# Performance work log

Measured on AMD Instinct MI355X. Metric: run time of the kernel, lower is better.

Reference implementation:

```python
import jax, jax.numpy as jnp
import numpy as np


def setup_inputs() -> dict:
    key = jax.random.key(0)
    ks = jax.random.split(key, 8)
    B, C, H, W = 16, 192, 64, 64
    dt_rank, d_state = 12, 1
    return {
        "x": jax.random.normal(ks[0], (B, C, H, W), dtype=jnp.float32),
        "conv_w": jax.random.normal(ks[1], (C, 1, 5, 5), dtype=jnp.float32) * 0.1,
        "conv_b": jax.random.normal(ks[2], (C,), dtype=jnp.float32) * 0.1,
        "x_proj_w": jax.random.normal(ks[3], (dt_rank + 2 * d_state, C), dtype=jnp.float32) * (C ** -0.5),
        "dt_w": jax.random.normal(ks[4], (C, dt_rank), dtype=jnp.float32) * (dt_rank ** -0.5),
        "dt_b": jax.random.normal(ks[5], (C,), dtype=jnp.float32) * 0.1,
        "A_logs": jnp.zeros((C, d_state), dtype=jnp.float32),  # log(arange(1,d_state+1)) with d_state=1 -> 0
        "Ds": jnp.ones((C,), dtype=jnp.float32),
    }


def reference(x, conv_w, conv_b, x_proj_w, dt_w, dt_b, A_logs, Ds):
    B, C, H, W = x.shape
    L = H * W
    dt_rank = dt_w.shape[1]
    n = A_logs.shape[1]  # d_state
    # depthwise conv2d, kernel 5, padding SAME (=d_conv//2), then SiLU
    x = jax.lax.conv_general_dilated(
        x, conv_w, window_strides=(1, 1), padding='SAME',
        feature_group_count=C, dimension_numbers=('NCHW', 'OIHW', 'NCHW'))
    x = jax.nn.silu(x + conv_b[None, :, None, None])
    xs = x.reshape(B, C, L)  # (b, d, l)
    # x_proj: (dt_rank + 2n, C) @ (b, C, l)
    x_dbl = jnp.einsum('kc,bcl->bkl', x_proj_w, xs)
    dts, Bs, Cs = jnp.split(x_dbl, [dt_rank, dt_rank + n], axis=1)
    # dt projection + softplus (delta_softplus=True with delta_bias)
    delta = jax.nn.softplus(jnp.einsum('cr,brl->bcl', dt_w, dts) + dt_b[None, :, None])  # (b,d,l)
    A = -jnp.exp(A_logs)  # (d, n)
    # selective scan returning the full state trajectory h_t (b,d,n,l):
    # h_t = exp(delta_t * A) * h_{t-1} + delta_t * B_t * u_t
    a = jnp.exp(delta[:, :, None, :] * A[None, :, :, None])        # (b,d,n,l)
    b_el = delta[:, :, None, :] * Bs[:, None, :, :] * xs[:, :, None, :]  # (b,d,n,l)

    def combine(e1, e2):
        a1, b1 = e1
        a2, b2 = e2
        return (a1 * a2, a2 * b1 + b2)

    _, h = jax.lax.associative_scan(combine, (a, b_el), axis=-1)  # h: (b,d,n,l)
    state = h.reshape(B, C * n, L)
    # y = C_t * h_t + D * u (fp32, d_state=1 broadcast)
    y = state.astype(jnp.float32) * Cs.astype(jnp.float32) + xs * Ds[:, None]
    return y.reshape(B, C, H, W)
```

## Files before the change

kernel.cpp:

```cpp
#include <hip/hip_runtime.h>
#include <hip/hip_bf16.h>
#include <cstddef>

#define BB 16
#define CC 192
#define HH 64
#define WW 64
#define LL 4096
#define DTR 12
#define KK 14

__device__ __forceinline__ float silu_f(float v) {
  return v / (1.f + __expf(-v));
}

__global__ __launch_bounds__(256) void conv_silu_kernel(
    const float* __restrict__ x, const float* __restrict__ cw,
    const float* __restrict__ cb, float* __restrict__ xs) {
  const int bc = blockIdx.x;
  const int c = bc % CC;
  const int tid = threadIdx.x;
  const int lane = tid & 63;
  const int wv = tid >> 6;
  const int oy0 = wv * 16;

  float w[25];
#pragma unroll
  for (int k = 0; k < 25; ++k) w[k] = cw[c * 25 + k];
  const float bias = cb[c];

  const float* xp = x + (size_t)bc * LL + lane;
  float* op = xs + (size_t)bc * LL + lane;

  float rv[20];
#pragma unroll
  for (int r = 0; r < 20; ++r) {
    const int gr = oy0 + r - 2;
    float v = 0.f;
    if ((unsigned)gr < 64u) v = xp[gr * 64];
    rv[r] = v;
  }

  float acc[5];
#pragma unroll
  for (int i = 0; i < 5; ++i) acc[i] = 0.f;

#pragma unroll
  for (int r = 0; r < 20; ++r) {
    float v = rv[r];
    float vm2 = __shfl_up(v, 2u, 64);
    float vm1 = __shfl_up(v, 1u, 64);
    float vp1 = __shfl_down(v, 1u, 64);
    float vp2 = __shfl_down(v, 2u, 64);
    if (lane < 2) vm2 = 0.f;
    if (lane < 1) vm1 = 0.f;
    if (lane > 62) vp1 = 0.f;
    if (lane > 61) vp2 = 0.f;
    float t[5] = {vm2, vm1, v, vp1, vp2};
#pragma unroll
    for (int ky = 0; ky < 5; ++ky) {
      if (r >= ky && (r - ky) < 16) {
        float s = acc[(r - ky) % 5];
#pragma unroll
        for (int kx = 0; kx < 5; ++kx) s += w[ky * 5 + kx] * t[kx];
        acc[(r - ky) % 5] = s;
      }
    }
    if (r >= 4) {
      const int yf = oy0 + r - 4;
      float a = acc[(r - 4) % 5] + bias;
      op[yf * 64] = silu_f(a);
      acc[(r - 4) % 5] = 0.f;
    }
  }
}

__global__ __launch_bounds__(896) void proj_kernel(
    const float* __restrict__ xs, const float* __restrict__ xpw,
    float* __restrict__ xdbl) {
  const int b = blockIdx.y;
  const int l0 = blockIdx.x * 128;
  const int tid = threadIdx.x;
  const int lane = tid & 63;
  const int k = tid >> 6;

  const float* bp = xs + (size_t)b * CC * LL + l0 + lane * 2;
  const float* wp = xpw + k * CC;
  float ax = 0.f, ay = 0.f;
#pragma unroll 8
  for (int c = 0; c < CC; ++c) {
    const float2 v = *(const float2*)(bp + (size_t)c * LL);
    const float w = wp[c];
    ax += w * v.x;
    ay += w * v.y;
  }
  *(float2*)(xdbl + ((size_t)b * KK + k) * LL + l0 + lane * 2) =
      make_float2(ax, ay);
}

__global__ __launch_bounds__(512) void scan_kernel(
    const float* __restrict__ xs, const float* __restrict__ xdbl,
    const float* __restrict__ dtw, const float* __restrict__ dtb,
    const float* __restrict__ A_logs, const float* __restrict__ Ds,
    float* __restrict__ y) {
  const int bc = blockIdx.x;
  const int b = bc / CC;
  const int c = bc - b * CC;
  const int tid = threadIdx.x;
  const int lane = tid & 63;
  const int wv = tid >> 6;

  const float Ac = -__expf(A_logs[c]);
  const float Dc = Ds[c];
  float dw[DTR];
#pragma unroll
  for (int r = 0; r < DTR; ++r) dw[r] = dtw[c * DTR + r];
  const float db = dtb[c];

  const float* xp = xs + (size_t)bc * LL;
  const float* xb = xdbl + (size_t)b * KK * LL;
  float* yp = y + (size_t)bc * LL;

  __shared__ float segA[8];
  __shared__ float segB[8];

  float alpha[8], beta[8];
  float aggA[2], aggB[2];

#pragma unroll
  for (int ck = 0; ck < 2; ++ck) {
    const int base = wv * 512 + ck * 256 + lane * 4;
    const float4 x4 = *(const float4*)(xp + base);
    const float4 B4 = *(const float4*)(xb + 12 * LL + base);
    const float4 C4 = *(const float4*)(xb + 13 * LL + base);
    float zx = db, zy = db, zz_ = db, zw = db;
#pragma unroll
    for (int r = 0; r < DTR; ++r) {
      const float4 d4 = *(const float4*)(xb + r * LL + base);
      zx += dw[r] * d4.x;
      zy += dw[r] * d4.y;
      zz_ += dw[r] * d4.z;
      zw += dw[r] * d4.w;
    }
    const float zq[4] = {zx, zy, zz_, zw};
    float Pl = 1.f, hl = 0.f;
#pragma unroll
    for (int q = 0; q < 4; ++q) {
      const float z = zq[q];
      const float delta = (z > 15.f) ? z : __logf(1.f + __expf(z));
      const float a = __expf(delta * Ac);
      const float be = delta * ((&B4.x)[q]) * ((&x4.x)[q]);
      hl = a * hl + be;
      Pl = Pl * a;
      alpha[ck * 4 + q] = Pl * ((&C4.x)[q]);
      beta[ck * 4 + q] = hl * ((&C4.x)[q]) + ((&x4.x)[q]) * Dc;
    }
    aggA[ck] = Pl;
    aggB[ck] = hl;
  }

  float iA[2], iB[2];
#pragma unroll
  for (int ck = 0; ck < 2; ++ck) { iA[ck] = aggA[ck]; iB[ck] = aggB[ck]; }
#pragma unroll
  for (int s = 1; s < 64; s <<= 1) {
    float pA[2], pB[2];
#pragma unroll
    for (int ck = 0; ck < 2; ++ck) {
      pA[ck] = __shfl_up(iA[ck], (unsigned)s, 64);
      pB[ck] = __shfl_up(iB[ck], (unsigned)s, 64);
    }
    if (lane >= s) {
#pragma unroll
      for (int ck = 0; ck < 2; ++ck) {
        iB[ck] = iA[ck] * pB[ck] + iB[ck];
        iA[ck] = iA[ck] * pA[ck];
      }
    }
  }
  float eA[2], eB[2], tA[2], tB[2];
#pragma unroll
  for (int ck = 0; ck < 2; ++ck) {
    eA[ck] = __shfl_up(iA[ck], 1u, 64);
    eB[ck] = __shfl_up(iB[ck], 1u, 64);
    if (lane == 0) { eA[ck] = 1.f; eB[ck] = 0.f; }
    tA[ck] = __shfl(iA[ck], 63, 64);
    tB[ck] = __shfl(iB[ck], 63, 64);
  }

  float Pe[2], he[2];
  float SP = 1.f, Sh = 0.f;
#pragma unroll
  for (int ck = 0; ck < 2; ++ck) {
    Pe[ck] = SP * eA[ck];
    he[ck] = eA[ck] * Sh + eB[ck];
    Sh = tA[ck] * Sh + tB[ck];
    SP = SP * tA[ck];
  }

  if (lane == 0) { segA[wv] = SP; segB[wv] = Sh; }
  __syncthreads();
  float carry = 0.f;
  for (int i = 0; i < wv; ++i) carry = segA[i] * carry + segB[i];

#pragma unroll
  for (int ck = 0; ck < 2; ++ck) {
    const float G = Pe[ck] * carry + he[ck];
    const int base = wv * 512 + ck * 256 + lane * 4;
    float4 o;
    o.x = alpha[ck * 4 + 0] * G + beta[ck * 4 + 0];
    o.y = alpha[ck * 4 + 1] * G + beta[ck * 4 + 1];
    o.z = alpha[ck * 4 + 2] * G + beta[ck * 4 + 2];
    o.w = alpha[ck * 4 + 3] * G + beta[ck * 4 + 3];
    *(float4*)(yp + base) = o;
  }
}

extern "C" void kernel_launch(void* const* d_in, const int* in_sizes, int n_in,
                              void* d_out, int out_size, void* d_ws,
                              size_t ws_size, hipStream_t stream) {
  const float* x        = (const float*)d_in[0];
  const float* conv_w   = (const float*)d_in[1];
  const float* conv_b   = (const float*)d_in[2];
  const float* x_proj_w = (const float*)d_in[3];
  const float* dt_w     = (const float*)d_in[4];
  const float* dt_b     = (const float*)d_in[5];
  const float* A_logs   = (const float*)d_in[6];
  const float* Ds       = (const float*)d_in[7];
  float* out = (float*)d_out;

  char* ws = (char*)d_ws;
  const size_t plane_bytes = (size_t)BB * CC * LL * sizeof(float);
  float* xs   = (float*)ws;
  float* xdbl = (float*)(ws + plane_bytes);

  conv_silu_kernel<<<dim3(BB * CC), 256, 0, stream>>>(x, conv_w, conv_b, xs);
  proj_kernel<<<dim3(LL / 128, BB), 896, 0, stream>>>(xs, x_proj_w, xdbl);
  scan_kernel<<<dim3(BB * CC), 512, 0, stream>>>(xs, xdbl, dt_w, dt_b,
                                                 A_logs, Ds, out);
}
```

Baseline: 204.8 us.

## Split x_proj over channel slices with register-blocked partials and a reduce pass

```diff
diff --git a/kernel.cpp b/kernel.cpp
--- a/kernel.cpp
+++ b/kernel.cpp
@@ -9,6 +9,7 @@
 #define LL 4096
 #define DTR 12
 #define KK 14
+#define NSL 8
 
 __device__ __forceinline__ float silu_f(float v) {
   return v / (1.f + __expf(-v));
@@ -75,27 +76,55 @@
   }
 }
 
-__global__ __launch_bounds__(896) void proj_kernel(
+__global__ __launch_bounds__(64) void proj_part_kernel(
     const float* __restrict__ xs, const float* __restrict__ xpw,
-    float* __restrict__ xdbl) {
+    float* __restrict__ part) {
+  const int l0 = blockIdx.x * 256;
   const int b = blockIdx.y;
-  const int l0 = blockIdx.x * 128;
-  const int tid = threadIdx.x;
-  const int lane = tid & 63;
-  const int k = tid >> 6;
-
-  const float* bp = xs + (size_t)b * CC * LL + l0 + lane * 2;
-  const float* wp = xpw + k * CC;
-  float ax = 0.f, ay = 0.f;
-#pragma unroll 8
-  for (int c = 0; c < CC; ++c) {
-    const float2 v = *(const float2*)(bp + (size_t)c * LL);
-    const float w = wp[c];
-    ax += w * v.x;
-    ay += w * v.y;
-  }
-  *(float2*)(xdbl + ((size_t)b * KK + k) * LL + l0 + lane * 2) =
-      make_float2(ax, ay);
+  const int sl = blockIdx.z;
+  const int lane = threadIdx.x;
+  const int c0 = sl * 24;
+
+  float4 acc[KK];
+#pragma unroll
+  for (int k = 0; k < KK; ++k) acc[k] = make_float4(0.f, 0.f, 0.f, 0.f);
+
+  const float* bp = xs + ((size_t)(b * CC + c0)) * LL + l0 + lane * 4;
+#pragma unroll 6
+  for (int cc = 0; cc < 24; ++cc) {
+    const float4 v = *(const float4*)(bp + (size_t)cc * LL);
+    const int c = c0 + cc;
+#pragma unroll
+    for (int k = 0; k < KK; ++k) {
+      const float w = xpw[k * CC + c];
+      acc[k].x += w * v.x;
+      acc[k].y += w * v.y;
+      acc[k].z += w * v.z;
+      acc[k].w += w * v.w;
+    }
+  }
+
+  float* pp = part + ((size_t)((b * NSL + sl) * KK)) * LL + l0 + lane * 4;
+#pragma unroll
+  for (int k = 0; k < KK; ++k)
+    *(float4*)(pp + (size_t)k * LL) = acc[k];
+}
+
+__global__ __launch_bounds__(256) void proj_reduce_kernel(
+    const float* __restrict__ part, float* __restrict__ xdbl) {
+  const int f = blockIdx.x * 256 + threadIdx.x;
+  const int k = blockIdx.y;
+  const int b = blockIdx.z;
+  const size_t off = (size_t)f * 4;
+
+  float4 s = make_float4(0.f, 0.f, 0.f, 0.f);
+#pragma unroll
+  for (int sl = 0; sl < NSL; ++sl) {
+    const float4 v = *(const float4*)(
+        part + ((size_t)((b * NSL + sl) * KK + k)) * LL + off);
+    s.x += v.x; s.y += v.y; s.z += v.z; s.w += v.w;
+  }
+  *(float4*)(xdbl + ((size_t)(b * KK + k)) * LL + off) = s;
 }
 
 __global__ __launch_bounds__(512) void scan_kernel(
@@ -231,11 +260,16 @@
 
   char* ws = (char*)d_ws;
   const size_t plane_bytes = (size_t)BB * CC * LL * sizeof(float);
+  const size_t xdbl_bytes  = (size_t)BB * KK * LL * sizeof(float);
   float* xs   = (float*)ws;
   float* xdbl = (float*)(ws + plane_bytes);
+  float* part = (float*)(ws + plane_bytes + xdbl_bytes);
 
   conv_silu_kernel<<<dim3(BB * CC), 256, 0, stream>>>(x, conv_w, conv_b, xs);
-  proj_kernel<<<dim3(LL / 128, BB), 896, 0, stream>>>(xs, x_proj_w, xdbl);
+  proj_part_kernel<<<dim3(LL / 256, BB, NSL), 64, 0, stream>>>(
+      xs, x_proj_w, part);
+  proj_reduce_kernel<<<dim3(LL / 4 / 256, KK, BB), 256, 0, stream>>>(
+      part, xdbl);
   scan_kernel<<<dim3(BB * CC), 512, 0, stream>>>(xs, xdbl, dt_w, dt_b,
                                                  A_logs, Ds, out);
 }
```

Measured after the change: 174.9 us. 1.17x faster.
